# Kernel optimization log

Hardware: AMD Instinct MI355X
Metric: run time of the kernel (lower is better)

The kernel has to match this reference:

```python
import jax, jax.numpy as jnp
import numpy as np

N, E, D, L = 50000, 800000, 128, 3

def setup_inputs() -> dict:
    key = jax.random.key(0)
    ks = jax.random.split(key, 6)
    X = jax.random.normal(ks[0], (N, D), dtype=jnp.float32)
    edge_index = jax.random.randint(ks[1], (2, E), 0, N, dtype=jnp.int64)
    eps = jax.random.normal(ks[2], (L,), dtype=jnp.float32)
    # Glorot-ish scaling for stability
    W1 = jax.random.normal(ks[3], (L, D, D), dtype=jnp.float32) / np.sqrt(D)
    b1 = jnp.zeros((L, D), dtype=jnp.float32)
    W2 = jax.random.normal(ks[4], (L, D, D), dtype=jnp.float32) / np.sqrt(D)
    b2 = jnp.zeros((L, D), dtype=jnp.float32)
    return {"X": X, "edge_index": edge_index, "eps": eps,
            "W1": W1, "b1": b1, "W2": W2, "b2": b2}

def reference(X, edge_index, eps, W1, b1, W2, b2):
    src = edge_index[0]  # message sources j (flow source_to_target)
    dst = edge_index[1]  # aggregation targets i
    n = X.shape[0]
    for i in range(L):  # fixed small layer loop
        X0 = X
        # propagate: gather X_j over edges, scatter-add to targets
        S = jax.ops.segment_sum(X[src], dst, num_segments=n)  # [N, D]
        Z = (1.0 + eps[i]) * X + S
        # MLP: Linear -> ReLU -> Linear
        H = jnp.maximum(Z @ W1[i] + b1[i], 0.0)
        X = H @ W2[i] + b2[i]
        X = X + X0  # residual=True
    return X
```

## Files before the change

### kernel.cpp

```cpp
#include <hip/hip_runtime.h>

#define NN 50000
#define NE 800000
#define DD 128
#define NL 3
#define ELLW 64
#define MT_TOTAL (NN / 16)
#define EDGE_BLKS ((NE + 255) / 256)
#define PACK_BLKS ((6 * 2048 * 8 + 2047) / 2048)
#define INIT_BLKS ((NN * DD / 8 + 255) / 256)

typedef short bf16x8 __attribute__((ext_vector_type(8)));
typedef float f32x4 __attribute__((ext_vector_type(4)));
typedef _Float16 half8 __attribute__((ext_vector_type(8)));
typedef unsigned short u16x8 __attribute__((ext_vector_type(8)));

__device__ __forceinline__ unsigned short f2bf(float x) {
  unsigned u = __float_as_uint(x);
  u += 0x7FFFu + ((u >> 16) & 1u);
  return (unsigned short)(u >> 16);
}
__device__ __forceinline__ float bf2f(unsigned short h) {
  return __uint_as_float(((unsigned)h) << 16);
}
__device__ __forceinline__ void cvt8(const float* zz, bf16x8* hi, bf16x8* lo) {
#pragma unroll
  for (int i = 0; i < 8; ++i) {
    unsigned short h = f2bf(zz[i]);
    (*hi)[i] = (short)h;
    (*lo)[i] = (short)f2bf(zz[i] - bf2f(h));
  }
}

__global__ __launch_bounds__(256) void prologue_k(
    const int* __restrict__ ei, int* __restrict__ cnt, unsigned short* __restrict__ ell,
    const float* __restrict__ W1, const float* __restrict__ W2,
    unsigned short* __restrict__ Wp,
    const float* __restrict__ X, _Float16* __restrict__ Xh)
{
  int b = blockIdx.x;
  if (b < EDGE_BLKS) {
    int e = b * 256 + threadIdx.x;
    if (e < NE) {
      int s = ei[e];
      int d = ei[NE + e];
      int pos = atomicAdd(&cnt[d], 1);
      if (pos < ELLW) ell[(size_t)d * ELLW + pos] = (unsigned short)s;
    }
  } else if (b < EDGE_BLKS + PACK_BLKS) {
    int t = (b - EDGE_BLKS) * 256 + threadIdx.x;
    if (t < 6 * 2048) {
      int m = t >> 11;
      int rem = t & 2047;
      int l = rem & 63;
      int ntks = rem >> 6;
      int ks = ntks & 3, nt = ntks >> 2;
      const float* W = (m < 3) ? (W1 + (size_t)m * DD * DD) : (W2 + (size_t)(m - 3) * DD * DD);
      int col = nt * 16 + (l & 15);
      int k0 = ks * 32 + (l >> 4) * 8;
      unsigned short* hi = Wp + (size_t)m * 2 * DD * DD + (size_t)rem * 8;
      unsigned short* lo = hi + DD * DD;
#pragma unroll
      for (int i = 0; i < 8; ++i) {
        float w = W[(size_t)(k0 + i) * DD + col];
        unsigned short h = f2bf(w);
        hi[i] = h;
        lo[i] = f2bf(w - bf2f(h));
      }
    }
  } else {
    int t = (b - EDGE_BLKS - PACK_BLKS) * 256 + threadIdx.x;
    if (t < NN * DD / 8) {
      const float4* p = (const float4*)X + (size_t)t * 2;
      float4 a = p[0], bb = p[1];
      half8 h;
      h[0] = (_Float16)a.x;  h[1] = (_Float16)a.y;  h[2] = (_Float16)a.z;  h[3] = (_Float16)a.w;
      h[4] = (_Float16)bb.x; h[5] = (_Float16)bb.y; h[6] = (_Float16)bb.z; h[7] = (_Float16)bb.w;
      *(half8*)(Xh + (size_t)t * 8) = h;
    }
  }
}

template<int SELF_F32, int OUT_F32>
__global__ __launch_bounds__(256) void fused_layer_k(
    const float* __restrict__ Xf_in, const _Float16* __restrict__ Xh_in,
    const int* __restrict__ cnt, const unsigned short* __restrict__ ell,
    const float* __restrict__ eps, int layer,
    const unsigned short* __restrict__ Wp1, const float* __restrict__ b1,
    const unsigned short* __restrict__ Wp2, const float* __restrict__ b2,
    float* __restrict__ Xf_out, _Float16* __restrict__ Xh_out)
{
  __shared__ float ztile[2][16 * 132];
  __shared__ unsigned short rtile[2][16 * 136];
  const int w = threadIdx.x >> 6, l = threadIdx.x & 63;
  const int pair = w >> 1, h = w & 1;
  const int mt = blockIdx.x * 2 + pair;
  const bool active = (mt < MT_TOTAL);
  const int c = l & 15, grp = l >> 4;
  float* my = ztile[pair];
  unsigned short* rz = rtile[pair];

  if (active) {
    const float e1 = 1.0f + eps[layer];
#pragma unroll
    for (int pass = 0; pass < 2; ++pass) {
      int nl = h * 8 + pass * 4 + grp;
      int node = mt * 16 + nl;
      int deg = cnt[node]; deg = deg > ELLW ? ELLW : deg;
      const unsigned short* el = ell + (size_t)node * ELLW;
      float acc[8];
      if (SELF_F32) {
        const float* xr = Xf_in + (size_t)node * DD + c * 8;
        float4 a0 = *(const float4*)xr, a1 = *(const float4*)(xr + 4);
        float sv[8] = {a0.x, a0.y, a0.z, a0.w, a1.x, a1.y, a1.z, a1.w};
        u16x8 rb;
#pragma unroll
        for (int i = 0; i < 8; ++i) {
          acc[i] = e1 * sv[i];
          _Float16 hh = (_Float16)sv[i];
          rb[i] = *(unsigned short*)&hh;
        }
        *(u16x8*)(rz + nl * 136 + c * 8) = rb;
      } else {
        half8 sv = *(const half8*)(Xh_in + (size_t)node * DD + c * 8);
#pragma unroll
        for (int i = 0; i < 8; ++i) acc[i] = e1 * (float)sv[i];
        *(u16x8*)(rz + nl * 136 + c * 8) = *(const u16x8*)&sv;
      }
      int nf8 = deg >> 3;
      const u16x8* el8 = (const u16x8*)el;
      u16x8 nxt;
      if (nf8) nxt = el8[0];
      for (int t = 0; t < nf8; ++t) {
        u16x8 cur = nxt;
        if (t + 1 < nf8) nxt = el8[t + 1];
        half8 v0 = *(const half8*)(Xh_in + (size_t)cur[0] * DD + c * 8);
        half8 v1 = *(const half8*)(Xh_in + (size_t)cur[1] * DD + c * 8);
        half8 v2 = *(const half8*)(Xh_in + (size_t)cur[2] * DD + c * 8);
        half8 v3 = *(const half8*)(Xh_in + (size_t)cur[3] * DD + c * 8);
        half8 v4 = *(const half8*)(Xh_in + (size_t)cur[4] * DD + c * 8);
        half8 v5 = *(const half8*)(Xh_in + (size_t)cur[5] * DD + c * 8);
        half8 v6 = *(const half8*)(Xh_in + (size_t)cur[6] * DD + c * 8);
        half8 v7 = *(const half8*)(Xh_in + (size_t)cur[7] * DD + c * 8);
#pragma unroll
        for (int i = 0; i < 8; ++i)
          acc[i] += (((float)v0[i] + (float)v1[i]) + ((float)v2[i] + (float)v3[i]))
                  + (((float)v4[i] + (float)v5[i]) + ((float)v6[i] + (float)v7[i]));
      }
      for (int j = nf8 * 8; j < deg; ++j) {
        half8 v = *(const half8*)(Xh_in + (size_t)el[j] * DD + c * 8);
#pragma unroll
        for (int i = 0; i < 8; ++i) acc[i] += (float)v[i];
      }
      float* dst = my + nl * 132 + c * 8;
      *(float4*)dst = make_float4(acc[0], acc[1], acc[2], acc[3]);
      *(float4*)(dst + 4) = make_float4(acc[4], acc[5], acc[6], acc[7]);
    }
  }
  __syncthreads();

  f32x4 acc1[4];
#pragma unroll
  for (int nt = 0; nt < 4; ++nt) acc1[nt] = (f32x4){0.f, 0.f, 0.f, 0.f};
  if (active) {
    const float* arow = my + (l & 15) * 132;
    const unsigned short* Whi = Wp1;
    const unsigned short* Wlo = Wp1 + DD * DD;
#pragma unroll
    for (int ks = 0; ks < 4; ++ks) {
      const float* zp = arow + ks * 32 + grp * 8;
      float zz[8] = {zp[0], zp[1], zp[2], zp[3], zp[4], zp[5], zp[6], zp[7]};
      bf16x8 ahi, alo; cvt8(zz, &ahi, &alo);
#pragma unroll
      for (int nt = 0; nt < 4; ++nt) {
        int ntb = h * 4 + nt;
        size_t off = ((size_t)(ntb * 4 + ks) * 64 + l) * 8;
        bf16x8 bhi = *(const bf16x8*)(Whi + off);
        bf16x8 blo = *(const bf16x8*)(Wlo + off);
        acc1[nt] = __builtin_amdgcn_mfma_f32_16x16x32_bf16(ahi, bhi, acc1[nt], 0, 0, 0);
        acc1[nt] = __builtin_amdgcn_mfma_f32_16x16x32_bf16(ahi, blo, acc1[nt], 0, 0, 0);
        acc1[nt] = __builtin_amdgcn_mfma_f32_16x16x32_bf16(alo, bhi, acc1[nt], 0, 0, 0);
      }
    }
  }
  __syncthreads();

  if (active) {
#pragma unroll
    for (int nt = 0; nt < 4; ++nt) {
      int ntb = h * 4 + nt;
      float bv = b1[ntb * 16 + c];
#pragma unroll
      for (int r = 0; r < 4; ++r)
        my[(grp * 4 + r) * 132 + ntb * 16 + c] = fmaxf(acc1[nt][r] + bv, 0.f);
    }
  }
  __syncthreads();

  f32x4 acc2[4];
#pragma unroll
  for (int nt = 0; nt < 4; ++nt) acc2[nt] = (f32x4){0.f, 0.f, 0.f, 0.f};
  if (active) {
    const float* arow = my + (l & 15) * 132;
    const unsigned short* Whi = Wp2;
    const unsigned short* Wlo = Wp2 + DD * DD;
#pragma unroll
    for (int ks = 0; ks < 4; ++ks) {
      const float* hp = arow + ks * 32 + grp * 8;
      float hh[8] = {hp[0], hp[1], hp[2], hp[3], hp[4], hp[5], hp[6], hp[7]};
      bf16x8 ahi, alo; cvt8(hh, &ahi, &alo);
#pragma unroll
      for (int nt = 0; nt < 4; ++nt) {
        int ntb = h * 4 + nt;
        size_t off = ((size_t)(ntb * 4 + ks) * 64 + l) * 8;
        bf16x8 bhi = *(const bf16x8*)(Whi + off);
        bf16x8 blo = *(const bf16x8*)(Wlo + off);
        acc2[nt] = __builtin_amdgcn_mfma_f32_16x16x32_bf16(ahi, bhi, acc2[nt], 0, 0, 0);
        acc2[nt] = __builtin_amdgcn_mfma_f32_16x16x32_bf16(ahi, blo, acc2[nt], 0, 0, 0);
        acc2[nt] = __builtin_amdgcn_mfma_f32_16x16x32_bf16(alo, bhi, acc2[nt], 0, 0, 0);
      }
    }
#pragma unroll
    for (int nt = 0; nt < 4; ++nt) {
      int ntb = h * 4 + nt;
      int col = ntb * 16 + c;
      float bv = b2[col];
#pragma unroll
      for (int r = 0; r < 4; ++r) {
        int row = grp * 4 + r;
        int node = mt * 16 + row;
        size_t idx = (size_t)node * DD + col;
        unsigned short rb = rz[row * 136 + col];
        float rv = (float)(*(_Float16*)&rb);
        float v = acc2[nt][r] + bv + rv;
        if (OUT_F32) Xf_out[idx] = v;
        else         Xh_out[idx] = (_Float16)v;
      }
    }
  }
}

extern "C" void kernel_launch(void* const* d_in, const int* in_sizes, int n_in,
                              void* d_out, int out_size, void* d_ws, size_t ws_size,
                              hipStream_t stream) {
  const float* X   = (const float*)d_in[0];
  const int*   ei  = (const int*)d_in[1];
  const float* eps = (const float*)d_in[2];
  const float* W1  = (const float*)d_in[3];
  const float* b1  = (const float*)d_in[4];
  const float* W2  = (const float*)d_in[5];
  const float* b2  = (const float*)d_in[6];
  float* Xout = (float*)d_out;

  char* ws = (char*)d_ws;
  size_t off = 0;
  int* cnt = (int*)(ws + off); off += 256 * (((size_t)NN * 4 + 255) / 256);
  unsigned short* ell = (unsigned short*)(ws + off); off += (size_t)NN * ELLW * 2;
  unsigned short* Wp = (unsigned short*)(ws + off); off += (size_t)6 * 2 * DD * DD * 2;
  off = 256 * ((off + 255) / 256);
  _Float16* Xh0 = (_Float16*)(ws + off); off += (size_t)NN * DD * 2;
  _Float16* Xh1 = (_Float16*)(ws + off); off += (size_t)NN * DD * 2;

  hipMemsetAsync(cnt, 0, NN * 4, stream);
  prologue_k<<<EDGE_BLKS + PACK_BLKS + INIT_BLKS, 256, 0, stream>>>(
      ei, cnt, ell, W1, W2, Wp, X, Xh0);

  const int fgrid = (MT_TOTAL + 1) / 2;
  fused_layer_k<1, 0><<<fgrid, 256, 0, stream>>>(X, Xh0, cnt, ell, eps, 0,
      Wp + (size_t)0 * 2 * DD * DD, b1 + 0 * DD,
      Wp + (size_t)3 * 2 * DD * DD, b2 + 0 * DD, nullptr, Xh1);
  fused_layer_k<0, 0><<<fgrid, 256, 0, stream>>>(nullptr, Xh1, cnt, ell, eps, 1,
      Wp + (size_t)1 * 2 * DD * DD, b1 + 1 * DD,
      Wp + (size_t)4 * 2 * DD * DD, b2 + 1 * DD, nullptr, Xh0);
  fused_layer_k<0, 1><<<fgrid, 256, 0, stream>>>(nullptr, Xh0, cnt, ell, eps, 2,
      Wp + (size_t)2 * 2 * DD * DD, b1 + 2 * DD,
      Wp + (size_t)5 * 2 * DD * DD, b2 + 2 * DD, Xout, nullptr);
}
```

Before: 212.9 us.

## Replace fixed-width ELL adjacency with CSR built by count, scan, scatter

Builds the adjacency as compact CSR: count in-degrees, take an exclusive scan in a single-block kernel, then scatter source indices. The fused layers now read row_ptr/csr instead of a 64-wide ELL, which drops the degree cap of 64 and the large, sparsely filled ELL buffer. Layer 0 now reads the fp16 copy of X for its self term instead of the fp32 input, so its residual and self term lose precision. The cost is two extra launches, including a serial 1024-thread scan, and unaligned scalar index loads in place of 16-byte vector index loads.

```diff
diff --git a/kernel.cpp b/kernel.cpp
--- a/kernel.cpp
+++ b/kernel.cpp
@@ -4,10 +4,9 @@
 #define NE 800000
 #define DD 128
 #define NL 3
-#define ELLW 64
 #define MT_TOTAL (NN / 16)
 #define EDGE_BLKS ((NE + 255) / 256)
-#define PACK_BLKS ((6 * 2048 * 8 + 2047) / 2048)
+#define PACK_BLKS ((6 * 2048 + 255) / 256)
 #define INIT_BLKS ((NN * DD / 8 + 255) / 256)
 
 typedef short bf16x8 __attribute__((ext_vector_type(8)));
@@ -32,8 +31,8 @@
   }
 }
 
-__global__ __launch_bounds__(256) void prologue_k(
-    const int* __restrict__ ei, int* __restrict__ cnt, unsigned short* __restrict__ ell,
+__global__ __launch_bounds__(256) void phase1_k(
+    const int* __restrict__ ei, int* __restrict__ cnt,
     const float* __restrict__ W1, const float* __restrict__ W2,
     unsigned short* __restrict__ Wp,
     const float* __restrict__ X, _Float16* __restrict__ Xh)
@@ -41,12 +40,7 @@
   int b = blockIdx.x;
   if (b < EDGE_BLKS) {
     int e = b * 256 + threadIdx.x;
-    if (e < NE) {
-      int s = ei[e];
-      int d = ei[NE + e];
-      int pos = atomicAdd(&cnt[d], 1);
-      if (pos < ELLW) ell[(size_t)d * ELLW + pos] = (unsigned short)s;
-    }
+    if (e < NE) atomicAdd(&cnt[ei[NE + e]], 1);
   } else if (b < EDGE_BLKS + PACK_BLKS) {
     int t = (b - EDGE_BLKS) * 256 + threadIdx.x;
     if (t < 6 * 2048) {
@@ -81,10 +75,46 @@
   }
 }
 
-template<int SELF_F32, int OUT_F32>
+__global__ __launch_bounds__(1024) void scan_k(const int* __restrict__ cnt,
+                                               int* __restrict__ row_ptr,
+                                               int* __restrict__ wpos) {
+  __shared__ int part[1024];
+  const int T = 1024, C = (NN + T - 1) / T;
+  int t = threadIdx.x;
+  int base = t * C;
+  int s = 0;
+  for (int i = 0; i < C; ++i) { int idx = base + i; if (idx < NN) s += cnt[idx]; }
+  part[t] = s;
+  __syncthreads();
+  for (int off = 1; off < T; off <<= 1) {
+    int v = (t >= off) ? part[t - off] : 0;
+    __syncthreads();
+    if (t >= off) part[t] += v;
+    __syncthreads();
+  }
+  int run = (t > 0) ? part[t - 1] : 0;
+  for (int i = 0; i < C; ++i) {
+    int idx = base + i;
+    if (idx < NN) { row_ptr[idx] = run; wpos[idx] = run; run += cnt[idx]; }
+  }
+  if (t == T - 1) row_ptr[NN] = part[T - 1];
+}
+
+__global__ __launch_bounds__(256) void scatter_k(const int* __restrict__ ei,
+                                                 int* __restrict__ wpos,
+                                                 unsigned short* __restrict__ csr) {
+  int e = blockIdx.x * 256 + threadIdx.x;
+  if (e >= NE) return;
+  int s = ei[e];
+  int d = ei[NE + e];
+  int p = atomicAdd(&wpos[d], 1);
+  csr[p] = (unsigned short)s;
+}
+
+template<int OUT_F32>
 __global__ __launch_bounds__(256) void fused_layer_k(
-    const float* __restrict__ Xf_in, const _Float16* __restrict__ Xh_in,
-    const int* __restrict__ cnt, const unsigned short* __restrict__ ell,
+    const _Float16* __restrict__ Xh_in,
+    const int* __restrict__ row_ptr, const unsigned short* __restrict__ csr,
     const float* __restrict__ eps, int layer,
     const unsigned short* __restrict__ Wp1, const float* __restrict__ b1,
     const unsigned short* __restrict__ Wp2, const float* __restrict__ b2,
@@ -106,42 +136,29 @@
     for (int pass = 0; pass < 2; ++pass) {
       int nl = h * 8 + pass * 4 + grp;
       int node = mt * 16 + nl;
-      int deg = cnt[node]; deg = deg > ELLW ? ELLW : deg;
-      const unsigned short* el = ell + (size_t)node * ELLW;
+      int start = row_ptr[node];
+      int deg = row_ptr[node + 1] - start;
+      const unsigned short* el = csr + start;
       float acc[8];
-      if (SELF_F32) {
-        const float* xr = Xf_in + (size_t)node * DD + c * 8;
-        float4 a0 = *(const float4*)xr, a1 = *(const float4*)(xr + 4);
-        float sv[8] = {a0.x, a0.y, a0.z, a0.w, a1.x, a1.y, a1.z, a1.w};
-        u16x8 rb;
-#pragma unroll
-        for (int i = 0; i < 8; ++i) {
-          acc[i] = e1 * sv[i];
-          _Float16 hh = (_Float16)sv[i];
-          rb[i] = *(unsigned short*)&hh;
-        }
-        *(u16x8*)(rz + nl * 136 + c * 8) = rb;
-      } else {
+      {
         half8 sv = *(const half8*)(Xh_in + (size_t)node * DD + c * 8);
 #pragma unroll
         for (int i = 0; i < 8; ++i) acc[i] = e1 * (float)sv[i];
         *(u16x8*)(rz + nl * 136 + c * 8) = *(const u16x8*)&sv;
       }
       int nf8 = deg >> 3;
-      const u16x8* el8 = (const u16x8*)el;
-      u16x8 nxt;
-      if (nf8) nxt = el8[0];
       for (int t = 0; t < nf8; ++t) {
-        u16x8 cur = nxt;
-        if (t + 1 < nf8) nxt = el8[t + 1];
-        half8 v0 = *(const half8*)(Xh_in + (size_t)cur[0] * DD + c * 8);
-        half8 v1 = *(const half8*)(Xh_in + (size_t)cur[1] * DD + c * 8);
-        half8 v2 = *(const half8*)(Xh_in + (size_t)cur[2] * DD + c * 8);
-        half8 v3 = *(const half8*)(Xh_in + (size_t)cur[3] * DD + c * 8);
-        half8 v4 = *(const half8*)(Xh_in + (size_t)cur[4] * DD + c * 8);
-        half8 v5 = *(const half8*)(Xh_in + (size_t)cur[5] * DD + c * 8);
-        half8 v6 = *(const half8*)(Xh_in + (size_t)cur[6] * DD + c * 8);
-        half8 v7 = *(const half8*)(Xh_in + (size_t)cur[7] * DD + c * 8);
+        const unsigned short* ip = el + t * 8;
+        int i0 = ip[0], i1 = ip[1], i2 = ip[2], i3 = ip[3];
+        int i4 = ip[4], i5 = ip[5], i6 = ip[6], i7 = ip[7];
+        half8 v0 = *(const half8*)(Xh_in + (size_t)i0 * DD + c * 8);
+        half8 v1 = *(const half8*)(Xh_in + (size_t)i1 * DD + c * 8);
+        half8 v2 = *(const half8*)(Xh_in + (size_t)i2 * DD + c * 8);
+        half8 v3 = *(const half8*)(Xh_in + (size_t)i3 * DD + c * 8);
+        half8 v4 = *(const half8*)(Xh_in + (size_t)i4 * DD + c * 8);
+        half8 v5 = *(const half8*)(Xh_in + (size_t)i5 * DD + c * 8);
+        half8 v6 = *(const half8*)(Xh_in + (size_t)i6 * DD + c * 8);
+        half8 v7 = *(const half8*)(Xh_in + (size_t)i7 * DD + c * 8);
 #pragma unroll
         for (int i = 0; i < 8; ++i)
           acc[i] += (((float)v0[i] + (float)v1[i]) + ((float)v2[i] + (float)v3[i]))
@@ -254,25 +271,28 @@
 
   char* ws = (char*)d_ws;
   size_t off = 0;
-  int* cnt = (int*)(ws + off); off += 256 * (((size_t)NN * 4 + 255) / 256);
-  unsigned short* ell = (unsigned short*)(ws + off); off += (size_t)NN * ELLW * 2;
-  unsigned short* Wp = (unsigned short*)(ws + off); off += (size_t)6 * 2 * DD * DD * 2;
+  int* cnt     = (int*)(ws + off); off += 256 * (((size_t)NN * 4 + 255) / 256);
+  int* row_ptr = (int*)(ws + off); off += 256 * (((size_t)(NN + 1) * 4 + 255) / 256);
+  int* wpos    = (int*)(ws + off); off += 256 * (((size_t)NN * 4 + 255) / 256);
+  unsigned short* csr = (unsigned short*)(ws + off); off += 256 * (((size_t)NE * 2 + 255) / 256);
+  unsigned short* Wp  = (unsigned short*)(ws + off); off += (size_t)6 * 2 * DD * DD * 2;
   off = 256 * ((off + 255) / 256);
   _Float16* Xh0 = (_Float16*)(ws + off); off += (size_t)NN * DD * 2;
   _Float16* Xh1 = (_Float16*)(ws + off); off += (size_t)NN * DD * 2;
 
   hipMemsetAsync(cnt, 0, NN * 4, stream);
-  prologue_k<<<EDGE_BLKS + PACK_BLKS + INIT_BLKS, 256, 0, stream>>>(
-      ei, cnt, ell, W1, W2, Wp, X, Xh0);
+  phase1_k<<<EDGE_BLKS + PACK_BLKS + INIT_BLKS, 256, 0, stream>>>(ei, cnt, W1, W2, Wp, X, Xh0);
+  scan_k<<<1, 1024, 0, stream>>>(cnt, row_ptr, wpos);
+  scatter_k<<<EDGE_BLKS, 256, 0, stream>>>(ei, wpos, csr);
 
   const int fgrid = (MT_TOTAL + 1) / 2;
-  fused_layer_k<1, 0><<<fgrid, 256, 0, stream>>>(X, Xh0, cnt, ell, eps, 0,
+  fused_layer_k<0><<<fgrid, 256, 0, stream>>>(Xh0, row_ptr, csr, eps, 0,
       Wp + (size_t)0 * 2 * DD * DD, b1 + 0 * DD,
       Wp + (size_t)3 * 2 * DD * DD, b2 + 0 * DD, nullptr, Xh1);
-  fused_layer_k<0, 0><<<fgrid, 256, 0, stream>>>(nullptr, Xh1, cnt, ell, eps, 1,
+  fused_layer_k<0><<<fgrid, 256, 0, stream>>>(Xh1, row_ptr, csr, eps, 1,
       Wp + (size_t)1 * 2 * DD * DD, b1 + 1 * DD,
       Wp + (size_t)4 * 2 * DD * DD, b2 + 1 * DD, nullptr, Xh0);
-  fused_layer_k<0, 1><<<fgrid, 256, 0, stream>>>(nullptr, Xh0, cnt, ell, eps, 2,
+  fused_layer_k<1><<<fgrid, 256, 0, stream>>>(Xh0, row_ptr, csr, eps, 2,
       Wp + (size_t)2 * 2 * DD * DD, b1 + 2 * DD,
       Wp + (size_t)5 * 2 * DD * DD, b2 + 2 * DD, Xout, nullptr);
 }
```

After: 365.8 us. 71.9% more time.

## Use one 16-node tile per block and read fp16 self features in layer 0

Applied to the files above, without the earlier changes.

Each 256-thread block now handles a single 16-node tile instead of two. All four waves share the gather, each wave doing one pass over 4 nodes, and in the MLP each wave computes 2 of the 8 output column tiles. Layer 0 now reads the fp16 copy of X for its self term and residual instead of the fp32 input, which drops the SELF_F32 template path. This doubles the grid, halves per-wave gather serialization and LDS per block, and reduces register pressure, but each wave now reloads the same A operands for fewer MFMA tiles. The layer-0 self and residual terms lose fp32 precision. The pack block count is also changed.

```diff
diff --git a/kernel.cpp b/kernel.cpp
--- a/kernel.cpp
+++ b/kernel.cpp
@@ -7,7 +7,7 @@
 #define ELLW 64
 #define MT_TOTAL (NN / 16)
 #define EDGE_BLKS ((NE + 255) / 256)
-#define PACK_BLKS ((6 * 2048 * 8 + 2047) / 2048)
+#define PACK_BLKS ((6 * 2048 + 255) / 256)
 #define INIT_BLKS ((NN * DD / 8 + 255) / 256)
 
 typedef short bf16x8 __attribute__((ext_vector_type(8)));
@@ -81,89 +81,70 @@
   }
 }
 
-template<int SELF_F32, int OUT_F32>
+template<int OUT_F32>
 __global__ __launch_bounds__(256) void fused_layer_k(
-    const float* __restrict__ Xf_in, const _Float16* __restrict__ Xh_in,
+    const _Float16* __restrict__ Xh_in,
     const int* __restrict__ cnt, const unsigned short* __restrict__ ell,
     const float* __restrict__ eps, int layer,
     const unsigned short* __restrict__ Wp1, const float* __restrict__ b1,
     const unsigned short* __restrict__ Wp2, const float* __restrict__ b2,
     float* __restrict__ Xf_out, _Float16* __restrict__ Xh_out)
 {
-  __shared__ float ztile[2][16 * 132];
-  __shared__ unsigned short rtile[2][16 * 136];
+  __shared__ float ztile[16 * 132];
+  __shared__ unsigned short rtile[16 * 136];
   const int w = threadIdx.x >> 6, l = threadIdx.x & 63;
-  const int pair = w >> 1, h = w & 1;
-  const int mt = blockIdx.x * 2 + pair;
-  const bool active = (mt < MT_TOTAL);
+  const int mt = blockIdx.x;
   const int c = l & 15, grp = l >> 4;
-  float* my = ztile[pair];
-  unsigned short* rz = rtile[pair];
-
-  if (active) {
+
+  {
     const float e1 = 1.0f + eps[layer];
-#pragma unroll
-    for (int pass = 0; pass < 2; ++pass) {
-      int nl = h * 8 + pass * 4 + grp;
-      int node = mt * 16 + nl;
-      int deg = cnt[node]; deg = deg > ELLW ? ELLW : deg;
-      const unsigned short* el = ell + (size_t)node * ELLW;
-      float acc[8];
-      if (SELF_F32) {
-        const float* xr = Xf_in + (size_t)node * DD + c * 8;
-        float4 a0 = *(const float4*)xr, a1 = *(const float4*)(xr + 4);
-        float sv[8] = {a0.x, a0.y, a0.z, a0.w, a1.x, a1.y, a1.z, a1.w};
-        u16x8 rb;
-#pragma unroll
-        for (int i = 0; i < 8; ++i) {
-          acc[i] = e1 * sv[i];
-          _Float16 hh = (_Float16)sv[i];
-          rb[i] = *(unsigned short*)&hh;
-        }
-        *(u16x8*)(rz + nl * 136 + c * 8) = rb;
-      } else {
-        half8 sv = *(const half8*)(Xh_in + (size_t)node * DD + c * 8);
-#pragma unroll
-        for (int i = 0; i < 8; ++i) acc[i] = e1 * (float)sv[i];
-        *(u16x8*)(rz + nl * 136 + c * 8) = *(const u16x8*)&sv;
-      }
-      int nf8 = deg >> 3;
-      const u16x8* el8 = (const u16x8*)el;
-      u16x8 nxt;
-      if (nf8) nxt = el8[0];
-      for (int t = 0; t < nf8; ++t) {
-        u16x8 cur = nxt;
-        if (t + 1 < nf8) nxt = el8[t + 1];
-        half8 v0 = *(const half8*)(Xh_in + (size_t)cur[0] * DD + c * 8);
-        half8 v1 = *(const half8*)(Xh_in + (size_t)cur[1] * DD + c * 8);
-        half8 v2 = *(const half8*)(Xh_in + (size_t)cur[2] * DD + c * 8);
-        half8 v3 = *(const half8*)(Xh_in + (size_t)cur[3] * DD + c * 8);
-        half8 v4 = *(const half8*)(Xh_in + (size_t)cur[4] * DD + c * 8);
-        half8 v5 = *(const half8*)(Xh_in + (size_t)cur[5] * DD + c * 8);
-        half8 v6 = *(const half8*)(Xh_in + (size_t)cur[6] * DD + c * 8);
-        half8 v7 = *(const half8*)(Xh_in + (size_t)cur[7] * DD + c * 8);
-#pragma unroll
-        for (int i = 0; i < 8; ++i)
-          acc[i] += (((float)v0[i] + (float)v1[i]) + ((float)v2[i] + (float)v3[i]))
-                  + (((float)v4[i] + (float)v5[i]) + ((float)v6[i] + (float)v7[i]));
-      }
-      for (int j = nf8 * 8; j < deg; ++j) {
-        half8 v = *(const half8*)(Xh_in + (size_t)el[j] * DD + c * 8);
-#pragma unroll
-        for (int i = 0; i < 8; ++i) acc[i] += (float)v[i];
-      }
-      float* dst = my + nl * 132 + c * 8;
-      *(float4*)dst = make_float4(acc[0], acc[1], acc[2], acc[3]);
-      *(float4*)(dst + 4) = make_float4(acc[4], acc[5], acc[6], acc[7]);
-    }
+    const int nl = w * 4 + grp;
+    const int node = mt * 16 + nl;
+    int deg = cnt[node]; deg = deg > ELLW ? ELLW : deg;
+    const unsigned short* el = ell + (size_t)node * ELLW;
+    const u16x8* el8 = (const u16x8*)el;
+    float acc[8];
+    {
+      half8 sv = *(const half8*)(Xh_in + (size_t)node * DD + c * 8);
+#pragma unroll
+      for (int i = 0; i < 8; ++i) acc[i] = e1 * (float)sv[i];
+      *(u16x8*)(rtile + nl * 136 + c * 8) = *(const u16x8*)&sv;
+    }
+    int nf8 = deg >> 3;
+    u16x8 nxt;
+    if (nf8) nxt = el8[0];
+    for (int t = 0; t < nf8; ++t) {
+      u16x8 cur = nxt;
+      if (t + 1 < nf8) nxt = el8[t + 1];
+      half8 v0 = *(const half8*)(Xh_in + (size_t)cur[0] * DD + c * 8);
+      half8 v1 = *(const half8*)(Xh_in + (size_t)cur[1] * DD + c * 8);
+      half8 v2 = *(const half8*)(Xh_in + (size_t)cur[2] * DD + c * 8);
+      half8 v3 = *(const half8*)(Xh_in + (size_t)cur[3] * DD + c * 8);
+      half8 v4 = *(const half8*)(Xh_in + (size_t)cur[4] * DD + c * 8);
+      half8 v5 = *(const half8*)(Xh_in + (size_t)cur[5] * DD + c * 8);
+      half8 v6 = *(const half8*)(Xh_in + (size_t)cur[6] * DD + c * 8);
+      half8 v7 = *(const half8*)(Xh_in + (size_t)cur[7] * DD + c * 8);
+#pragma unroll
+      for (int i = 0; i < 8; ++i)
+        acc[i] += (((float)v0[i] + (float)v1[i]) + ((float)v2[i] + (float)v3[i]))
+                + (((float)v4[i] + (float)v5[i]) + ((float)v6[i] + (float)v7[i]));
+    }
+    for (int j = nf8 * 8; j < deg; ++j) {
+      half8 v = *(const half8*)(Xh_in + (size_t)el[j] * DD + c * 8);
+#pragma unroll
+      for (int i = 0; i < 8; ++i) acc[i] += (float)v[i];
+    }
+    float* dst = ztile + nl * 132 + c * 8;
+    *(float4*)dst = make_float4(acc[0], acc[1], acc[2], acc[3]);
+    *(float4*)(dst + 4) = make_float4(acc[4], acc[5], acc[6], acc[7]);
   }
   __syncthreads();
 
-  f32x4 acc1[4];
-#pragma unroll
-  for (int nt = 0; nt < 4; ++nt) acc1[nt] = (f32x4){0.f, 0.f, 0.f, 0.f};
-  if (active) {
-    const float* arow = my + (l & 15) * 132;
+  f32x4 acc1[2];
+#pragma unroll
+  for (int nt = 0; nt < 2; ++nt) acc1[nt] = (f32x4){0.f, 0.f, 0.f, 0.f};
+  {
+    const float* arow = ztile + (l & 15) * 132;
     const unsigned short* Whi = Wp1;
     const unsigned short* Wlo = Wp1 + DD * DD;
 #pragma unroll
@@ -172,8 +153,8 @@
       float zz[8] = {zp[0], zp[1], zp[2], zp[3], zp[4], zp[5], zp[6], zp[7]};
       bf16x8 ahi, alo; cvt8(zz, &ahi, &alo);
 #pragma unroll
-      for (int nt = 0; nt < 4; ++nt) {
-        int ntb = h * 4 + nt;
+      for (int nt = 0; nt < 2; ++nt) {
+        int ntb = w * 2 + nt;
         size_t off = ((size_t)(ntb * 4 + ks) * 64 + l) * 8;
         bf16x8 bhi = *(const bf16x8*)(Whi + off);
         bf16x8 blo = *(const bf16x8*)(Wlo + off);
@@ -185,23 +166,23 @@
   }
   __syncthreads();
 
-  if (active) {
-#pragma unroll
-    for (int nt = 0; nt < 4; ++nt) {
-      int ntb = h * 4 + nt;
+  {
+#pragma unroll
+    for (int nt = 0; nt < 2; ++nt) {
+      int ntb = w * 2 + nt;
       float bv = b1[ntb * 16 + c];
 #pragma unroll
       for (int r = 0; r < 4; ++r)
-        my[(grp * 4 + r) * 132 + ntb * 16 + c] = fmaxf(acc1[nt][r] + bv, 0.f);
+        ztile[(grp * 4 + r) * 132 + ntb * 16 + c] = fmaxf(acc1[nt][r] + bv, 0.f);
     }
   }
   __syncthreads();
 
-  f32x4 acc2[4];
-#pragma unroll
-  for (int nt = 0; nt < 4; ++nt) acc2[nt] = (f32x4){0.f, 0.f, 0.f, 0.f};
-  if (active) {
-    const float* arow = my + (l & 15) * 132;
+  f32x4 acc2[2];
+#pragma unroll
+  for (int nt = 0; nt < 2; ++nt) acc2[nt] = (f32x4){0.f, 0.f, 0.f, 0.f};
+  {
+    const float* arow = ztile + (l & 15) * 132;
     const unsigned short* Whi = Wp2;
     const unsigned short* Wlo = Wp2 + DD * DD;
 #pragma unroll
@@ -210,8 +191,8 @@
       float hh[8] = {hp[0], hp[1], hp[2], hp[3], hp[4], hp[5], hp[6], hp[7]};
       bf16x8 ahi, alo; cvt8(hh, &ahi, &alo);
 #pragma unroll
-      for (int nt = 0; nt < 4; ++nt) {
-        int ntb = h * 4 + nt;
+      for (int nt = 0; nt < 2; ++nt) {
+        int ntb = w * 2 + nt;
         size_t off = ((size_t)(ntb * 4 + ks) * 64 + l) * 8;
         bf16x8 bhi = *(const bf16x8*)(Whi + off);
         bf16x8 blo = *(const bf16x8*)(Wlo + off);
@@ -221,8 +202,8 @@
       }
     }
 #pragma unroll
-    for (int nt = 0; nt < 4; ++nt) {
-      int ntb = h * 4 + nt;
+    for (int nt = 0; nt < 2; ++nt) {
+      int ntb = w * 2 + nt;
       int col = ntb * 16 + c;
       float bv = b2[col];
 #pragma unroll
@@ -230,7 +211,7 @@
         int row = grp * 4 + r;
         int node = mt * 16 + row;
         size_t idx = (size_t)node * DD + col;
-        unsigned short rb = rz[row * 136 + col];
+        unsigned short rb = rtile[row * 136 + col];
         float rv = (float)(*(_Float16*)&rb);
         float v = acc2[nt][r] + bv + rv;
         if (OUT_F32) Xf_out[idx] = v;
@@ -265,14 +246,14 @@
   prologue_k<<<EDGE_BLKS + PACK_BLKS + INIT_BLKS, 256, 0, stream>>>(
       ei, cnt, ell, W1, W2, Wp, X, Xh0);
 
-  const int fgrid = (MT_TOTAL + 1) / 2;
-  fused_layer_k<1, 0><<<fgrid, 256, 0, stream>>>(X, Xh0, cnt, ell, eps, 0,
+  const int fgrid = MT_TOTAL;
+  fused_layer_k<0><<<fgrid, 256, 0, stream>>>(Xh0, cnt, ell, eps, 0,
       Wp + (size_t)0 * 2 * DD * DD, b1 + 0 * DD,
       Wp + (size_t)3 * 2 * DD * DD, b2 + 0 * DD, nullptr, Xh1);
-  fused_layer_k<0, 0><<<fgrid, 256, 0, stream>>>(nullptr, Xh1, cnt, ell, eps, 1,
+  fused_layer_k<0><<<fgrid, 256, 0, stream>>>(Xh1, cnt, ell, eps, 1,
       Wp + (size_t)1 * 2 * DD * DD, b1 + 1 * DD,
       Wp + (size_t)4 * 2 * DD * DD, b2 + 1 * DD, nullptr, Xh0);
-  fused_layer_k<0, 1><<<fgrid, 256, 0, stream>>>(nullptr, Xh0, cnt, ell, eps, 2,
+  fused_layer_k<1><<<fgrid, 256, 0, stream>>>(Xh0, cnt, ell, eps, 2,
       Wp + (size_t)2 * 2 * DD * DD, b1 + 2 * DD,
       Wp + (size_t)5 * 2 * DD * DD, b2 + 2 * DD, Xout, nullptr);
 }
```

Measured after the change: 193.4 us. -9.2%, faster.
